# Performance work log

Hardware: AMD Instinct MI355X
Metric: run time of the kernel (lower is better)

The kernel has to match this reference:

```python
import jax, jax.numpy as jnp
import numpy as np
import math

N_NODES = 100000
N_EDGES = 1600000
DIM = 64

def setup_inputs() -> dict:
    key = jax.random.key(0)
    k_x, k_w, k_w1, k_row, k_col, k_dd = jax.random.split(key, 6)
    stdv = 1.0 / math.sqrt(DIM)
    X = jax.random.normal(k_x, (N_NODES, DIM), dtype=jnp.float32)
    W = jax.random.uniform(k_w, (DIM, DIM), dtype=jnp.float32, minval=-stdv, maxval=stdv)
    W1 = jax.random.uniform(k_w1, (DIM, DIM), dtype=jnp.float32, minval=-stdv, maxval=stdv)
    # CSR expansion of the graph: row_ids sorted (destination node of each edge)
    row_ids = jnp.sort(jax.random.randint(k_row, (N_EDGES,), 0, N_NODES, dtype=jnp.int32))
    col_ids = jax.random.randint(k_col, (N_EDGES,), 0, N_NODES, dtype=jnp.int32)
    # degree-like positive normalization vector, bounded away from 0
    dd1 = jax.random.uniform(k_dd, (N_NODES, 1), dtype=jnp.float32, minval=0.5, maxval=1.5)
    return {"X": X, "W": W, "W1": W1, "dd1": dd1, "row_ids": row_ids, "col_ids": col_ids}

def reference(X, W, W1, dd1, row_ids, col_ids):
    # X_prime = X @ W  (dense GEMM)
    XW = X @ W  # [N, D]
    # SpMM aggregation: out[i] = sum_{j in neighbors(i)} XW[j]
    agg = jax.ops.segment_sum(XW[col_ids], row_ids, num_segments=X.shape[0])  # [N, D]
    # per-node normalization + residual branch X @ W1
    return agg / dd1 + X @ W1
```

## Files before the change

kernel.cpp:

```cpp
#include <hip/hip_runtime.h>
#include <hip/hip_bf16.h>

#define DIMS 64
#define BATCH 16

typedef short  bf16x8 __attribute__((ext_vector_type(8)));
typedef float  f32x4v __attribute__((ext_vector_type(4)));

static __device__ __forceinline__ short f2bf(float f) {
    __hip_bfloat16 h = __float2bfloat16(f);
    return *reinterpret_cast<short*>(&h);
}

__global__ __launch_bounds__(256) void gcn_pre(
    const float* __restrict__ X, const float* __restrict__ W,
    const float* __restrict__ W1, __hip_bfloat16* __restrict__ XWh,
    __hip_bfloat16* __restrict__ XW1h, const int* __restrict__ rows,
    int* __restrict__ ptr, int N, int E, int gemmBlocks)
{
    if (blockIdx.x >= gemmBlocks) {
        const int rb = blockIdx.x - gemmBlocks;
        if (rb == 0 && threadIdx.x < 32)
            reinterpret_cast<uint32_t*>(XWh + ((size_t)N << 6))[threadIdx.x] = 0u;
        const int e = rb * 256 + threadIdx.x;
        if (e >= E) return;
        const int r1 = rows[e];
        const int r0 = (e == 0) ? -1 : rows[e - 1];
        for (int r = r0 + 1; r <= r1; ++r) ptr[r] = e;
        if (e == E - 1) {
            for (int r = r1 + 1; r <= N; ++r) ptr[r] = E;
        }
        return;
    }

    const int w    = threadIdx.x >> 6;
    const int lane = threadIdx.x & 63;
    const int L    = lane & 15;
    const int q    = lane >> 4;

    const int row0 = blockIdx.x * 64 + w * 16;
    const int rowA = row0 + L;
    const int rowC = (rowA < N) ? rowA : (N - 1);

    bf16x8 bfrag[2][2][4];
    #pragma unroll
    for (int kh = 0; kh < 2; ++kh)
        #pragma unroll
        for (int nt = 0; nt < 4; ++nt)
            #pragma unroll
            for (int j = 0; j < 8; ++j) {
                const int k = kh * 32 + q * 8 + j;
                bfrag[0][kh][nt][j] = f2bf(W [k * 64 + nt * 16 + L]);
                bfrag[1][kh][nt][j] = f2bf(W1[k * 64 + nt * 16 + L]);
            }

    f32x4v acc[2][4];
    #pragma unroll
    for (int m = 0; m < 2; ++m)
        #pragma unroll
        for (int nt = 0; nt < 4; ++nt)
            acc[m][nt] = (f32x4v){0.f, 0.f, 0.f, 0.f};

    #pragma unroll
    for (int kh = 0; kh < 2; ++kh) {
        const float4 xa = reinterpret_cast<const float4*>(
            X + (size_t)rowC * 64 + kh * 32 + q * 8)[0];
        const float4 xb = reinterpret_cast<const float4*>(
            X + (size_t)rowC * 64 + kh * 32 + q * 8)[1];
        bf16x8 a;
        a[0] = f2bf(xa.x); a[1] = f2bf(xa.y); a[2] = f2bf(xa.z); a[3] = f2bf(xa.w);
        a[4] = f2bf(xb.x); a[5] = f2bf(xb.y); a[6] = f2bf(xb.z); a[7] = f2bf(xb.w);
        #pragma unroll
        for (int nt = 0; nt < 4; ++nt) {
            acc[0][nt] = __builtin_amdgcn_mfma_f32_16x16x32_bf16(
                a, bfrag[0][kh][nt], acc[0][nt], 0, 0, 0);
            acc[1][nt] = __builtin_amdgcn_mfma_f32_16x16x32_bf16(
                a, bfrag[1][kh][nt], acc[1][nt], 0, 0, 0);
        }
    }

    #pragma unroll
    for (int r = 0; r < 4; ++r) {
        const int row = row0 + q * 4 + r;
        if (row < N) {
            ushort4 p0, p1;
            p0.x = (unsigned short)f2bf(acc[0][0][r]);
            p0.y = (unsigned short)f2bf(acc[0][1][r]);
            p0.z = (unsigned short)f2bf(acc[0][2][r]);
            p0.w = (unsigned short)f2bf(acc[0][3][r]);
            p1.x = (unsigned short)f2bf(acc[1][0][r]);
            p1.y = (unsigned short)f2bf(acc[1][1][r]);
            p1.z = (unsigned short)f2bf(acc[1][2][r]);
            p1.w = (unsigned short)f2bf(acc[1][3][r]);
            *reinterpret_cast<ushort4*>(XWh  + ((size_t)row << 6) + 4 * L) = p0;
            *reinterpret_cast<ushort4*>(XW1h + ((size_t)row << 6) + 4 * L) = p1;
        }
    }
}

__global__ __launch_bounds__(256) void gcn_csr(
    const __hip_bfloat16* __restrict__ XWh, const __hip_bfloat16* __restrict__ XW1h,
    const float* __restrict__ dd1, const int* __restrict__ ptr,
    const int* __restrict__ cols, float* __restrict__ out, int N, int E)
{
    const int t    = blockIdx.x * 256 + threadIdx.x;
    const int wave = t >> 6;
    const int lane = threadIdx.x & 63;
    const int g    = lane >> 3;
    const int d    = lane & 7;

    const int row = wave * 8 + g;
    int p0 = 0, p1 = 0;
    if (row < N) { p0 = ptr[row]; p1 = ptr[row + 1]; }

    float acc[8];
    #pragma unroll
    for (int k = 0; k < 8; ++k) acc[k] = 0.f;

    for (int e = p0; __any(e < p1); e += BATCH) {
        uint4 raw[BATCH];
        #pragma unroll
        for (int j = 0; j < BATCH; ++j) {
            const int ee = e + j;
            const int es = (ee < E) ? ee : (E - 1);
            const int cl = cols[es];
            const int c  = (ee < p1) ? cl : N;
            raw[j] = *reinterpret_cast<const uint4*>(
                XWh + (((size_t)c) << 6) + (d << 3));
        }
        #pragma unroll
        for (int j = 0; j < BATCH; ++j) {
            const uint32_t w0 = raw[j].x, w1 = raw[j].y, w2 = raw[j].z, w3 = raw[j].w;
            acc[0] += __uint_as_float(w0 << 16);
            acc[1] += __uint_as_float(w0 & 0xffff0000u);
            acc[2] += __uint_as_float(w1 << 16);
            acc[3] += __uint_as_float(w1 & 0xffff0000u);
            acc[4] += __uint_as_float(w2 << 16);
            acc[5] += __uint_as_float(w2 & 0xffff0000u);
            acc[6] += __uint_as_float(w3 << 16);
            acc[7] += __uint_as_float(w3 & 0xffff0000u);
        }
    }

    if (row < N) {
        const float s = 1.0f / dd1[row];
        const uint4 rr = *reinterpret_cast<const uint4*>(
            XW1h + (((size_t)row) << 6) + (d << 3));
        float res[8];
        res[0] = __uint_as_float(rr.x << 16);
        res[1] = __uint_as_float(rr.x & 0xffff0000u);
        res[2] = __uint_as_float(rr.y << 16);
        res[3] = __uint_as_float(rr.y & 0xffff0000u);
        res[4] = __uint_as_float(rr.z << 16);
        res[5] = __uint_as_float(rr.z & 0xffff0000u);
        res[6] = __uint_as_float(rr.w << 16);
        res[7] = __uint_as_float(rr.w & 0xffff0000u);
        #pragma unroll
        for (int tt = 0; tt < 4; ++tt) {
            float2 o;
            o.x = acc[tt]     * s + res[tt];
            o.y = acc[4 + tt] * s + res[4 + tt];
            *reinterpret_cast<float2*>(
                out + ((size_t)row << 6) + tt * 16 + d * 2) = o;
        }
    }
}

extern "C" void kernel_launch(void* const* d_in, const int* in_sizes, int n_in,
                              void* d_out, int out_size, void* d_ws, size_t ws_size,
                              hipStream_t stream) {
    const float* X   = (const float*)d_in[0];
    const float* W   = (const float*)d_in[1];
    const float* W1  = (const float*)d_in[2];
    const float* dd1 = (const float*)d_in[3];
    const int* rows  = (const int*)d_in[4];
    const int* cols  = (const int*)d_in[5];

    const int N = in_sizes[3];
    const int E = in_sizes[4];

    char* wsp = (char*)d_ws;
    __hip_bfloat16* XWh = (__hip_bfloat16*)wsp;
    size_t off = (((size_t)(N + 1) * DIMS * sizeof(__hip_bfloat16)) + 255) & ~(size_t)255;
    __hip_bfloat16* XW1h = (__hip_bfloat16*)(wsp + off);
    off += (((size_t)N * DIMS * sizeof(__hip_bfloat16)) + 255) & ~(size_t)255;
    int* row_ptr = (int*)(wsp + off);

    float* out = (float*)d_out;

    const int gemmBlocks = (N + 63) / 64;
    const int rptrBlocks = (E + 255) / 256;
    hipLaunchKernelGGL(gcn_pre, dim3(gemmBlocks + rptrBlocks), dim3(256), 0, stream,
                       X, W, W1, XWh, XW1h, rows, row_ptr, N, E, gemmBlocks);

    const int waves  = (N + 7) / 8;
    const int blocks = (waves + 3) / 4;
    hipLaunchKernelGGL(gcn_csr, dim3(blocks), dim3(256), 0, stream,
                       XWh, XW1h, dd1, row_ptr, cols, out, N, E);
}
```

Measured before the change: 133.3 us.

## Process two row tiles per GEMM wave and tune the CSR gather loop

The GEMM kernel now has each wave handle two 16-row tiles (128 rows per block), so the converted W/W1 fragments are reused and both X tiles are loaded before the MFMAs. In the CSR kernel the gather batch drops from 16 to 8, and accumulation uses packed float2 vectors to allow packed FP32 adds. The dd1 and residual loads are hoisted ahead of the edge loop, gather addresses use 32-bit byte offsets, and output stores are nontemporal. These changes target register pressure, fragment setup overhead and latency, but a smaller batch means fewer loads in flight per wave.

```diff
diff --git a/kernel.cpp b/kernel.cpp
--- a/kernel.cpp
+++ b/kernel.cpp
@@ -2,10 +2,11 @@
 #include <hip/hip_bf16.h>
 
 #define DIMS 64
-#define BATCH 16
+#define BATCH 8
 
 typedef short  bf16x8 __attribute__((ext_vector_type(8)));
 typedef float  f32x4v __attribute__((ext_vector_type(4)));
+typedef float  f32x2v __attribute__((ext_vector_type(2)));
 
 static __device__ __forceinline__ short f2bf(float f) {
     __hip_bfloat16 h = __float2bfloat16(f);
@@ -38,9 +39,7 @@
     const int L    = lane & 15;
     const int q    = lane >> 4;
 
-    const int row0 = blockIdx.x * 64 + w * 16;
-    const int rowA = row0 + L;
-    const int rowC = (rowA < N) ? rowA : (N - 1);
+    const int row0 = blockIdx.x * 128 + w * 16;
 
     bf16x8 bfrag[2][2][4];
     #pragma unroll
@@ -54,46 +53,60 @@
                 bfrag[1][kh][nt][j] = f2bf(W1[k * 64 + nt * 16 + L]);
             }
 
-    f32x4v acc[2][4];
-    #pragma unroll
-    for (int m = 0; m < 2; ++m)
-        #pragma unroll
-        for (int nt = 0; nt < 4; ++nt)
-            acc[m][nt] = (f32x4v){0.f, 0.f, 0.f, 0.f};
-
-    #pragma unroll
-    for (int kh = 0; kh < 2; ++kh) {
-        const float4 xa = reinterpret_cast<const float4*>(
-            X + (size_t)rowC * 64 + kh * 32 + q * 8)[0];
-        const float4 xb = reinterpret_cast<const float4*>(
-            X + (size_t)rowC * 64 + kh * 32 + q * 8)[1];
-        bf16x8 a;
-        a[0] = f2bf(xa.x); a[1] = f2bf(xa.y); a[2] = f2bf(xa.z); a[3] = f2bf(xa.w);
-        a[4] = f2bf(xb.x); a[5] = f2bf(xb.y); a[6] = f2bf(xb.z); a[7] = f2bf(xb.w);
-        #pragma unroll
-        for (int nt = 0; nt < 4; ++nt) {
-            acc[0][nt] = __builtin_amdgcn_mfma_f32_16x16x32_bf16(
-                a, bfrag[0][kh][nt], acc[0][nt], 0, 0, 0);
-            acc[1][nt] = __builtin_amdgcn_mfma_f32_16x16x32_bf16(
-                a, bfrag[1][kh][nt], acc[1][nt], 0, 0, 0);
-        }
-    }
-
-    #pragma unroll
-    for (int r = 0; r < 4; ++r) {
-        const int row = row0 + q * 4 + r;
-        if (row < N) {
-            ushort4 p0, p1;
-            p0.x = (unsigned short)f2bf(acc[0][0][r]);
-            p0.y = (unsigned short)f2bf(acc[0][1][r]);
-            p0.z = (unsigned short)f2bf(acc[0][2][r]);
-            p0.w = (unsigned short)f2bf(acc[0][3][r]);
-            p1.x = (unsigned short)f2bf(acc[1][0][r]);
-            p1.y = (unsigned short)f2bf(acc[1][1][r]);
-            p1.z = (unsigned short)f2bf(acc[1][2][r]);
-            p1.w = (unsigned short)f2bf(acc[1][3][r]);
-            *reinterpret_cast<ushort4*>(XWh  + ((size_t)row << 6) + 4 * L) = p0;
-            *reinterpret_cast<ushort4*>(XW1h + ((size_t)row << 6) + 4 * L) = p1;
+    float4 xr[2][2][2];
+    #pragma unroll
+    for (int t = 0; t < 2; ++t) {
+        const int rowA = row0 + t * 64 + L;
+        const int rowC = (rowA < N) ? rowA : (N - 1);
+        const float* xp = X + (size_t)rowC * 64;
+        #pragma unroll
+        for (int kh = 0; kh < 2; ++kh) {
+            xr[t][kh][0] = reinterpret_cast<const float4*>(xp + kh * 32 + q * 8)[0];
+            xr[t][kh][1] = reinterpret_cast<const float4*>(xp + kh * 32 + q * 8)[1];
+        }
+    }
+
+    #pragma unroll
+    for (int t = 0; t < 2; ++t) {
+        f32x4v acc[2][4];
+        #pragma unroll
+        for (int m = 0; m < 2; ++m)
+            #pragma unroll
+            for (int nt = 0; nt < 4; ++nt)
+                acc[m][nt] = (f32x4v){0.f, 0.f, 0.f, 0.f};
+
+        #pragma unroll
+        for (int kh = 0; kh < 2; ++kh) {
+            const float4 xa = xr[t][kh][0];
+            const float4 xb = xr[t][kh][1];
+            bf16x8 a;
+            a[0] = f2bf(xa.x); a[1] = f2bf(xa.y); a[2] = f2bf(xa.z); a[3] = f2bf(xa.w);
+            a[4] = f2bf(xb.x); a[5] = f2bf(xb.y); a[6] = f2bf(xb.z); a[7] = f2bf(xb.w);
+            #pragma unroll
+            for (int nt = 0; nt < 4; ++nt) {
+                acc[0][nt] = __builtin_amdgcn_mfma_f32_16x16x32_bf16(
+                    a, bfrag[0][kh][nt], acc[0][nt], 0, 0, 0);
+                acc[1][nt] = __builtin_amdgcn_mfma_f32_16x16x32_bf16(
+                    a, bfrag[1][kh][nt], acc[1][nt], 0, 0, 0);
+            }
+        }
+
+        #pragma unroll
+        for (int r = 0; r < 4; ++r) {
+            const int row = row0 + t * 64 + q * 4 + r;
+            if (row < N) {
+                ushort4 p0, p1;
+                p0.x = (unsigned short)f2bf(acc[0][0][r]);
+                p0.y = (unsigned short)f2bf(acc[0][1][r]);
+                p0.z = (unsigned short)f2bf(acc[0][2][r]);
+                p0.w = (unsigned short)f2bf(acc[0][3][r]);
+                p1.x = (unsigned short)f2bf(acc[1][0][r]);
+                p1.y = (unsigned short)f2bf(acc[1][1][r]);
+                p1.z = (unsigned short)f2bf(acc[1][2][r]);
+                p1.w = (unsigned short)f2bf(acc[1][3][r]);
+                *reinterpret_cast<ushort4*>(XWh  + ((size_t)row << 6) + 4 * L) = p0;
+                *reinterpret_cast<ushort4*>(XW1h + ((size_t)row << 6) + 4 * L) = p1;
+            }
         }
     }
 }
@@ -111,11 +124,19 @@
 
     const int row = wave * 8 + g;
     int p0 = 0, p1 = 0;
-    if (row < N) { p0 = ptr[row]; p1 = ptr[row + 1]; }
-
-    float acc[8];
-    #pragma unroll
-    for (int k = 0; k < 8; ++k) acc[k] = 0.f;
+    float s = 0.f;
+    uint4 rr = make_uint4(0u, 0u, 0u, 0u);
+    if (row < N) {
+        p0 = ptr[row];
+        p1 = ptr[row + 1];
+        s  = 1.0f / dd1[row];
+        rr = *reinterpret_cast<const uint4*>(
+            XW1h + (((size_t)row) << 6) + (d << 3));
+    }
+
+    f32x2v acc2[4];
+    #pragma unroll
+    for (int k = 0; k < 4; ++k) acc2[k] = (f32x2v){0.f, 0.f};
 
     for (int e = p0; __any(e < p1); e += BATCH) {
         uint4 raw[BATCH];
@@ -125,27 +146,31 @@
             const int es = (ee < E) ? ee : (E - 1);
             const int cl = cols[es];
             const int c  = (ee < p1) ? cl : N;
+            const uint32_t off = ((uint32_t)c << 7) + (uint32_t)(d << 4);
             raw[j] = *reinterpret_cast<const uint4*>(
-                XWh + (((size_t)c) << 6) + (d << 3));
+                reinterpret_cast<const char*>(XWh) + off);
         }
         #pragma unroll
         for (int j = 0; j < BATCH; ++j) {
-            const uint32_t w0 = raw[j].x, w1 = raw[j].y, w2 = raw[j].z, w3 = raw[j].w;
-            acc[0] += __uint_as_float(w0 << 16);
-            acc[1] += __uint_as_float(w0 & 0xffff0000u);
-            acc[2] += __uint_as_float(w1 << 16);
-            acc[3] += __uint_as_float(w1 & 0xffff0000u);
-            acc[4] += __uint_as_float(w2 << 16);
-            acc[5] += __uint_as_float(w2 & 0xffff0000u);
-            acc[6] += __uint_as_float(w3 << 16);
-            acc[7] += __uint_as_float(w3 & 0xffff0000u);
+            const uint32_t ww0 = raw[j].x, ww1 = raw[j].y,
+                           ww2 = raw[j].z, ww3 = raw[j].w;
+            f32x2v v0, v1, v2, v3;
+            v0.x = __uint_as_float(ww0 << 16);
+            v0.y = __uint_as_float(ww0 & 0xffff0000u);
+            v1.x = __uint_as_float(ww1 << 16);
+            v1.y = __uint_as_float(ww1 & 0xffff0000u);
+            v2.x = __uint_as_float(ww2 << 16);
+            v2.y = __uint_as_float(ww2 & 0xffff0000u);
+            v3.x = __uint_as_float(ww3 << 16);
+            v3.y = __uint_as_float(ww3 & 0xffff0000u);
+            acc2[0] += v0;
+            acc2[1] += v1;
+            acc2[2] += v2;
+            acc2[3] += v3;
         }
     }
 
     if (row < N) {
-        const float s = 1.0f / dd1[row];
-        const uint4 rr = *reinterpret_cast<const uint4*>(
-            XW1h + (((size_t)row) << 6) + (d << 3));
         float res[8];
         res[0] = __uint_as_float(rr.x << 16);
         res[1] = __uint_as_float(rr.x & 0xffff0000u);
@@ -155,13 +180,15 @@
         res[5] = __uint_as_float(rr.z & 0xffff0000u);
         res[6] = __uint_as_float(rr.w << 16);
         res[7] = __uint_as_float(rr.w & 0xffff0000u);
+        const float accs[8] = {acc2[0].x, acc2[0].y, acc2[1].x, acc2[1].y,
+                               acc2[2].x, acc2[2].y, acc2[3].x, acc2[3].y};
         #pragma unroll
         for (int tt = 0; tt < 4; ++tt) {
-            float2 o;
-            o.x = acc[tt]     * s + res[tt];
-            o.y = acc[4 + tt] * s + res[4 + tt];
-            *reinterpret_cast<float2*>(
-                out + ((size_t)row << 6) + tt * 16 + d * 2) = o;
+            f32x2v o;
+            o.x = accs[tt]     * s + res[tt];
+            o.y = accs[4 + tt] * s + res[4 + tt];
+            __builtin_nontemporal_store(o, reinterpret_cast<f32x2v*>(
+                out + ((size_t)row << 6) + tt * 16 + d * 2));
         }
     }
 }
@@ -188,7 +215,7 @@
 
     float* out = (float*)d_out;
 
-    const int gemmBlocks = (N + 63) / 64;
+    const int gemmBlocks = (N + 127) / 128;
     const int rptrBlocks = (E + 255) / 256;
     hipLaunchKernelGGL(gcn_pre, dim3(gemmBlocks + rptrBlocks), dim3(256), 0, stream,
                        X, W, W1, XWh, XW1h, rows, row_ptr, N, E, gemmBlocks);
```

Result: faster. 128.1 us (-3.9%).
